# Kernel tuning notes

Hardware: AMD Instinct MI355X
Metric: run time of the kernel (lower is better)

The kernel has to match this reference:

```python
import jax, jax.numpy as jnp
import numpy as np

# ModernBERT-base, local (sliding-window) attention layer (layer_id=1, global every 3)
B, S, H = 2, 4096, 768
NH, HD = 12, 64          # num heads, head dim
WINDOW = 128             # config.local_attention -> +/- WINDOW//2 tokens
ROPE_THETA = 10000.0     # local rope theta
NEG = jnp.float32(-1e9)


def setup_inputs() -> dict:
    key = jax.random.key(0)
    k1, k2, k3 = jax.random.split(key, 3)
    hidden_states = jax.random.normal(k1, (B, S, H), dtype=jnp.float32)
    Wqkv = jax.random.normal(k2, (3 * H, H), dtype=jnp.float32) * 0.02
    Wo = jax.random.normal(k3, (H, H), dtype=jnp.float32) * 0.02
    position_ids = jnp.broadcast_to(jnp.arange(S, dtype=jnp.int32), (B, S))
    # additive masks, [1,1,S,S] broadcast over batch/heads
    attention_mask = jnp.zeros((1, 1, S, S), dtype=jnp.float32)  # full attention (all visible)
    idx = jnp.arange(S)
    dist = jnp.abs(idx[:, None] - idx[None, :])
    sliding_window_mask = jnp.where(dist <= WINDOW // 2, 0.0, NEG).astype(jnp.float32)[None, None]
    return {
        "hidden_states": hidden_states,
        "attention_mask": attention_mask,
        "sliding_window_mask": sliding_window_mask,
        "position_ids": position_ids,
        "Wqkv": Wqkv,
        "Wo": Wo,
    }


def _rope_cos_sin(position_ids):
    inv_freq = 1.0 / (ROPE_THETA ** (jnp.arange(0, HD, 2, dtype=jnp.float32) / HD))  # [HD/2]
    freqs = position_ids.astype(jnp.float32)[..., None] * inv_freq  # [B,S,HD/2]
    emb = jnp.concatenate([freqs, freqs], axis=-1)  # [B,S,HD]
    return jnp.cos(emb), jnp.sin(emb)


def _rotate_half(x):
    x1, x2 = jnp.split(x, 2, axis=-1)
    return jnp.concatenate([-x2, x1], axis=-1)


def reference(hidden_states, attention_mask, sliding_window_mask, position_ids, Wqkv, Wo):
    qkv = jnp.einsum('bsh,oh->bso', hidden_states, Wqkv)  # [B,S,3H]
    q, k, v = jnp.split(qkv, 3, axis=-1)
    q = q.reshape(B, S, NH, HD)
    k = k.reshape(B, S, NH, HD)
    v = v.reshape(B, S, NH, HD)
    cos, sin = _rope_cos_sin(position_ids)  # [B,S,HD]
    cos, sin = cos[:, :, None, :], sin[:, :, None, :]
    q = q * cos + _rotate_half(q) * sin
    k = k * cos + _rotate_half(k) * sin
    # layer_id=1 -> sliding window (local) layer
    mask = sliding_window_mask
    scale = 1.0 / jnp.sqrt(jnp.float32(HD))
    scores = jnp.einsum('bqnd,bknd->bnqk', q, k) * scale + mask  # [B,NH,S,S]
    probs = jax.nn.softmax(scores, axis=-1)
    attn = jnp.einsum('bnqk,bknd->bqnd', probs, v).reshape(B, S, H)
    out = jnp.einsum('bsh,oh->bso', attn, Wo)  # dropout p=0 (eval)
    return out
```

## Files before the change

### kernel.cpp

```cpp
#include <hip/hip_runtime.h>
#include <hip/hip_bf16.h>
#include <math.h>

#define BB 2
#define SS 4096
#define HH 768
#define NHEADS 12
#define MTOT (BB*SS)
#define NQKV (3*HH)

typedef _Float16 f16;
typedef __attribute__((ext_vector_type(8))) _Float16 f16x8;
typedef __attribute__((ext_vector_type(4))) _Float16 f16x4;
typedef __attribute__((ext_vector_type(4))) float f32x4;

__device__ __forceinline__ void gld_lds16(const void* g, void* l) {
  __builtin_amdgcn_global_load_lds(
      (const __attribute__((address_space(1))) unsigned int*)g,
      (__attribute__((address_space(3))) unsigned int*)l, 16, 0, 0);
}

__global__ __launch_bounds__(256)
void cvt_all(const float* __restrict__ hs, const float* __restrict__ wq,
             const float* __restrict__ wo, f16* __restrict__ hs16,
             f16* __restrict__ wq16, f16* __restrict__ wo16) {
  const int n1 = MTOT * HH / 4, n2 = NQKV * HH / 4, n3 = HH * HH / 4;
  int i = blockIdx.x * 256 + threadIdx.x;
  const float* src;
  f16* dst;
  int j = i;
  if (i < n1) { src = hs; dst = hs16; }
  else if (i < n1 + n2) { src = wq; dst = wq16; j = i - n1; }
  else if (i < n1 + n2 + n3) { src = wo; dst = wo16; j = i - n1 - n2; }
  else return;
  float4 v = reinterpret_cast<const float4*>(src)[j];
  f16x4 o;
  o[0] = (f16)v.x; o[1] = (f16)v.y; o[2] = (f16)v.z; o[3] = (f16)v.w;
  reinterpret_cast<f16x4*>(dst)[j] = o;
}

__global__ void rope_table_kernel(float* __restrict__ ctab, float* __restrict__ stab) {
  int idx = blockIdx.x * 256 + threadIdx.x;
  if (idx >= SS * 32) return;
  int s = idx >> 5;
  int j = idx & 31;
  const double r = 0.7498942093324559;
  double inv = 1.0;
  for (int t = 0; t < j; ++t) inv *= r;
  double ph = (double)s * inv;
  const double TWO_PI = 6.283185307179586;
  double red = ph - TWO_PI * floor(ph / TWO_PI);
  float rf = (float)red;
  ctab[idx] = cosf(rf);
  stab[idx] = sinf(rf);
}

template<int EPI>
__global__ __launch_bounds__(256)
void gemm_f16(const f16* __restrict__ A, const f16* __restrict__ Bw,
              float* __restrict__ C,
              f16* __restrict__ Oq, f16* __restrict__ Ok, f16* __restrict__ Ov,
              const int* __restrict__ pos,
              const float* __restrict__ ctab, const float* __restrict__ stab,
              int Mtiles, int N, int K) {
  __shared__ __align__(16) f16 As[3][128][32];
  __shared__ __align__(16) f16 Bs[3][128][32];
  const int tid = threadIdx.x;
  const int lane = tid & 63;
  const int w = tid >> 6;
  const int wr = w >> 1, wc = w & 1;

  const int bid = blockIdx.x;
  const int xcd = bid & 7;
  const int idx = bid >> 3;
  const int mch = Mtiles >> 3;
  const int bm = (xcd * mch + (idx % mch)) * 128;
  const int bn = (idx / mch) * 128;

  f32x4 acc[4][4] = {};

  const int l4 = lane >> 2;
  const int lk = lane & 3;
  const int srow = w * 32;
  const int fr = lane & 15;
  const int fst = (l4 >> 1) & 3;
  const int pc = (((lane >> 4) ^ ((fr >> 1) & 3)) * 8);

  auto stage = [&](int buf, int k0) {
#pragma unroll
    for (int i = 0; i < 2; ++i) {
      int row = srow + i * 16 + l4;
      gld_lds16(A + (size_t)(bm + row) * K + k0 + (lk ^ fst) * 8,
                (char*)&As[0][0][0] + buf * 8192 + w * 2048 + i * 1024 + lane * 16);
      gld_lds16(Bw + (size_t)(bn + row) * K + k0 + (lk ^ fst) * 8,
                (char*)&Bs[0][0][0] + buf * 8192 + w * 2048 + i * 1024 + lane * 16);
    }
  };
  auto compute = [&](int buf) {
    f16x8 av[4], bv[4];
#pragma unroll
    for (int m = 0; m < 4; ++m)
      av[m] = *reinterpret_cast<const f16x8*>(&As[buf][wr * 64 + m * 16 + fr][pc]);
#pragma unroll
    for (int n = 0; n < 4; ++n)
      bv[n] = *reinterpret_cast<const f16x8*>(&Bs[buf][wc * 64 + n * 16 + fr][pc]);
    __builtin_amdgcn_s_setprio(1);
#pragma unroll
    for (int m = 0; m < 4; ++m)
#pragma unroll
      for (int n = 0; n < 4; ++n)
        acc[m][n] = __builtin_amdgcn_mfma_f32_16x16x32_f16(av[m], bv[n],
                                                           acc[m][n], 0, 0, 0);
    __builtin_amdgcn_s_setprio(0);
  };

  const int T = K >> 5;
  stage(0, 0);
  stage(1, 32);
  for (int t = 0; t < T; ++t) {
    if (t == T - 1)
      asm volatile("s_waitcnt vmcnt(0)" ::: "memory");
    else
      asm volatile("s_waitcnt vmcnt(4)" ::: "memory");
    __builtin_amdgcn_s_barrier();
    __builtin_amdgcn_sched_barrier(0);
    if (t + 2 < T) stage((t + 2) % 3, (t + 2) << 5);
    compute(t % 3);
  }

  const int cl = lane & 15;
  const int rg = lane >> 4;
  if (EPI == 0) {
#pragma unroll
    for (int m = 0; m < 4; ++m)
#pragma unroll
      for (int n = 0; n < 4; ++n)
#pragma unroll
        for (int r = 0; r < 4; ++r) {
          int row = bm + wr * 64 + m * 16 + rg * 4 + r;
          int col = bn + wc * 64 + n * 16 + cl;
          C[(size_t)row * N + col] = acc[m][n][r];
        }
  } else {
    const int sec = bn / HH;
    f16* dst = (sec == 0) ? Oq : ((sec == 1) ? Ok : Ov);
    const int hb = bn - sec * HH + wc * 64;
#pragma unroll
    for (int m = 0; m < 4; ++m)
#pragma unroll
      for (int r = 0; r < 4; ++r) {
        int row = bm + wr * 64 + m * 16 + rg * 4 + r;
        if (sec < 2) {
          int s = pos[row];
#pragma unroll
          for (int n = 0; n < 4; ++n) {
            int hd = hb + n * 16 + cl;
            int d = hd & 63;
            int d2 = d & 31;
            float c = ctab[s * 32 + d2];
            float sn = stab[s * 32 + d2];
            float val = acc[m][n][r];
            float pv = acc[m][n ^ 2][r];
            val = (d < 32) ? (val * c - pv * sn) : (val * c + pv * sn);
            if (sec == 0) val *= 0.125f;
            dst[(size_t)row * HH + hd] = (f16)val;
          }
        } else {
#pragma unroll
          for (int n = 0; n < 4; ++n)
            dst[(size_t)row * HH + hb + n * 16 + cl] = (f16)acc[m][n][r];
        }
      }
  }
}

#define AQT 64
#define AKT 192
#define KP 72
#define VPP 200

__global__ __launch_bounds__(256)
void attn_kernel(const f16* __restrict__ qg, const f16* __restrict__ kg,
                 const f16* __restrict__ vg, f16* __restrict__ og) {
  __shared__ __align__(16) f16 Ks[AKT][KP];
  __shared__ __align__(16) f16 Vs[64][192];
  __shared__ float sums[AQT];

  const int tid = threadIdx.x;
  const int lane = tid & 63;
  const int wq = tid >> 6;
  const int l15 = lane & 15, g = lane >> 4;
  const int lin = (blockIdx.x & 7) * 192 + (blockIdx.x >> 3);
  const int qt = lin & 63;
  const int h = (lin >> 6) % NHEADS;
  const int b = lin / (64 * NHEADS);
  const int q0 = qt * AQT;
  const int kbase = q0 - 64;

  const size_t qrow = ((size_t)(b * SS + q0 + wq * 16 + l15)) * HH + h * 64;
  const f16x8 bq0 = *reinterpret_cast<const f16x8*>(&qg[qrow + g * 8]);
  const f16x8 bq1 = *reinterpret_cast<const f16x8*>(&qg[qrow + 32 + g * 8]);

#pragma unroll
  for (int i = 0; i < 6; ++i) {
    int idx = tid + i * 256;
    int r = idx >> 3, ch = idx & 7;
    int kglob = kbase + r;
    f16x8 v = {};
    if (kglob >= 0 && kglob < SS)
      v = *reinterpret_cast<const f16x8*>(
          &kg[((size_t)(b * SS + kglob)) * HH + h * 64 + ch * 8]);
    *reinterpret_cast<f16x8*>(&Ks[r][ch * 8]) = v;
  }
#pragma unroll
  for (int i = 0; i < 6; ++i) {
    int idx = tid + i * 256;
    int r = idx >> 3, ch = idx & 7;
    int kglob = kbase + r;
    f16x8 v = {};
    if (kglob >= 0 && kglob < SS)
      v = *reinterpret_cast<const f16x8*>(
          &vg[((size_t)(b * SS + kglob)) * HH + h * 64 + ch * 8]);
    const int c = r >> 3, o = r & 7;
#pragma unroll
    for (int j = 0; j < 8; ++j) {
      const int row = ch * 8 + j;
      const int cp = c ^ (row & 7) ^ ((row >> 3) & 7);
      Vs[row][cp * 8 + o] = v[j];
    }
  }
  __syncthreads();

  f32x4 accs[12] = {};
#pragma unroll
  for (int f = 0; f < 12; ++f) {
    f16x8 ak = *reinterpret_cast<const f16x8*>(&Ks[f * 16 + l15][g * 8]);
    accs[f] = __builtin_amdgcn_mfma_f32_16x16x32_f16(ak, bq0, accs[f], 0, 0, 0);
  }
#pragma unroll
  for (int f = 0; f < 12; ++f) {
    f16x8 ak = *reinterpret_cast<const f16x8*>(&Ks[f * 16 + l15][32 + g * 8]);
    accs[f] = __builtin_amdgcn_mfma_f32_16x16x32_f16(ak, bq1, accs[f], 0, 0, 0);
  }
  __syncthreads();

  const int qloc = wq * 16 + l15;
  float mx = -1e30f;
#pragma unroll
  for (int f = 0; f < 12; ++f)
#pragma unroll
    for (int r = 0; r < 4; ++r) {
      int key = f * 16 + g * 4 + r;
      int kglob = kbase + key;
      bool valid = (key >= qloc) && (key <= qloc + 128) && (kglob >= 0) && (kglob < SS);
      float s = valid ? accs[f][r] : -1e30f;
      accs[f][r] = s;
      mx = fmaxf(mx, s);
    }
  mx = fmaxf(mx, __shfl_xor(mx, 16));
  mx = fmaxf(mx, __shfl_xor(mx, 32));
  f16* Ps = &Ks[0][0];
  float sum = 0.f;
#pragma unroll
  for (int f = 0; f < 12; ++f) {
    float p0 = __expf(accs[f][0] - mx);
    float p1 = __expf(accs[f][1] - mx);
    float p2 = __expf(accs[f][2] - mx);
    float p3 = __expf(accs[f][3] - mx);
    sum += (p0 + p1) + (p2 + p3);
    f16x4 pk;
    pk[0] = (f16)p0; pk[1] = (f16)p1; pk[2] = (f16)p2; pk[3] = (f16)p3;
    *reinterpret_cast<f16x4*>(&Ps[(size_t)qloc * VPP + f * 16 + g * 4]) = pk;
  }
  sum += __shfl_xor(sum, 16);
  sum += __shfl_xor(sum, 32);
  if (g == 0) sums[qloc] = sum;

  f32x4 acco[4] = {};
#pragma unroll
  for (int ks = 0; ks < 6; ++ks) {
    f16x8 pa = *reinterpret_cast<const f16x8*>(&Ps[(size_t)(wq * 16 + l15) * VPP + ks * 32 + g * 8]);
#pragma unroll
    for (int n = 0; n < 4; ++n) {
      const int row = n * 16 + l15;
      const int cp = (4 * ks + g) ^ (row & 7) ^ ((row >> 3) & 7);
      f16x8 bv = *reinterpret_cast<const f16x8*>(&Vs[row][cp * 8]);
      acco[n] = __builtin_amdgcn_mfma_f32_16x16x32_f16(pa, bv, acco[n], 0, 0, 0);
    }
  }
#pragma unroll
  for (int r = 0; r < 4; ++r) {
    int qo = wq * 16 + g * 4 + r;
    float inv = 1.0f / sums[qo];
    size_t base = ((size_t)(b * SS + q0 + qo)) * HH + h * 64;
#pragma unroll
    for (int n = 0; n < 4; ++n)
      og[base + n * 16 + l15] = (f16)(acco[n][r] * inv);
  }
}

extern "C" void kernel_launch(void* const* d_in, const int* in_sizes, int n_in,
                              void* d_out, int out_size, void* d_ws, size_t ws_size,
                              hipStream_t stream) {
  const float* hs = (const float*)d_in[0];
  const int* pos = (const int*)d_in[3];
  const float* Wqkv = (const float*)d_in[4];
  const float* Wo = (const float*)d_in[5];
  float* out = (float*)d_out;

  uint8_t* ws = (uint8_t*)d_ws;
  size_t off = 0;
  float* ctab = (float*)(ws + off); off += (size_t)SS * 32 * 4;
  float* stab = (float*)(ws + off); off += (size_t)SS * 32 * 4;
  f16* hs16 = (f16*)(ws + off); off += (size_t)MTOT * HH * 2;
  f16* wq16 = (f16*)(ws + off); off += (size_t)NQKV * HH * 2;
  f16* wo16 = (f16*)(ws + off); off += (size_t)HH * HH * 2;
  f16* qf = (f16*)(ws + off); off += (size_t)MTOT * HH * 2;
  f16* kf = (f16*)(ws + off); off += (size_t)MTOT * HH * 2;
  f16* vf = (f16*)(ws + off); off += (size_t)MTOT * HH * 2;
  f16* af = (f16*)(ws + off); off += (size_t)MTOT * HH * 2;

  const int ncvt = (MTOT * HH + NQKV * HH + HH * HH) / 4;
  cvt_all<<<(ncvt + 255) / 256, 256, 0, stream>>>(hs, Wqkv, Wo, hs16, wq16, wo16);
  rope_table_kernel<<<(SS * 32 + 255) / 256, 256, 0, stream>>>(ctab, stab);

  gemm_f16<1><<<(MTOT / 128) * (NQKV / 128), 256, 0, stream>>>(
      hs16, wq16, nullptr, qf, kf, vf, pos, ctab, stab, MTOT / 128, NQKV, HH);
  attn_kernel<<<BB * NHEADS * (SS / AQT), 256, 0, stream>>>(qf, kf, vf, af);
  gemm_f16<0><<<(MTOT / 128) * (HH / 128), 256, 0, stream>>>(
      af, wo16, out, nullptr, nullptr, nullptr, nullptr, nullptr, nullptr,
      MTOT / 128, HH, HH);
}
```

Before: 108.7 us.

## Load GEMM B operand directly into registers instead of staging through LDS

The weight (B) tiles in the f16 GEMM are now read straight from global memory into per-wave registers with double-buffered register sets. Only the A tiles still go through the triple-buffered LDS, which halves shared memory use and removes the B LDS reads. The cost is duplicated global loads of B across the two wave rows, more register pressure, and a new unrolled-by-two pipeline with different wait counts.

```diff
diff --git a/kernel.cpp b/kernel.cpp
--- a/kernel.cpp
+++ b/kernel.cpp
@@ -64,7 +64,6 @@
               const float* __restrict__ ctab, const float* __restrict__ stab,
               int Mtiles, int N, int K) {
   __shared__ __align__(16) f16 As[3][128][32];
-  __shared__ __align__(16) f16 Bs[3][128][32];
   const int tid = threadIdx.x;
   const int lane = tid & 63;
   const int w = tid >> 6;
@@ -83,27 +82,30 @@
   const int lk = lane & 3;
   const int srow = w * 32;
   const int fr = lane & 15;
+  const int g16 = lane >> 4;
   const int fst = (l4 >> 1) & 3;
-  const int pc = (((lane >> 4) ^ ((fr >> 1) & 3)) * 8);
-
-  auto stage = [&](int buf, int k0) {
+  const int pc = ((g16 ^ ((fr >> 1) & 3)) * 8);
+
+  const f16* bp = Bw + (size_t)(bn + wc * 64 + fr) * K + g16 * 8;
+
+  auto stageA = [&](int buf, int k0) {
 #pragma unroll
     for (int i = 0; i < 2; ++i) {
       int row = srow + i * 16 + l4;
       gld_lds16(A + (size_t)(bm + row) * K + k0 + (lk ^ fst) * 8,
                 (char*)&As[0][0][0] + buf * 8192 + w * 2048 + i * 1024 + lane * 16);
-      gld_lds16(Bw + (size_t)(bn + row) * K + k0 + (lk ^ fst) * 8,
-                (char*)&Bs[0][0][0] + buf * 8192 + w * 2048 + i * 1024 + lane * 16);
     }
   };
-  auto compute = [&](int buf) {
-    f16x8 av[4], bv[4];
+  auto loadB = [&](f16x8* breg, int k0) {
+#pragma unroll
+    for (int n = 0; n < 4; ++n)
+      breg[n] = *reinterpret_cast<const f16x8*>(bp + (size_t)n * 16 * K + k0);
+  };
+  auto compute = [&](int abuf, const f16x8* bv) {
+    f16x8 av[4];
 #pragma unroll
     for (int m = 0; m < 4; ++m)
-      av[m] = *reinterpret_cast<const f16x8*>(&As[buf][wr * 64 + m * 16 + fr][pc]);
-#pragma unroll
-    for (int n = 0; n < 4; ++n)
-      bv[n] = *reinterpret_cast<const f16x8*>(&Bs[buf][wc * 64 + n * 16 + fr][pc]);
+      av[m] = *reinterpret_cast<const f16x8*>(&As[abuf][wr * 64 + m * 16 + fr][pc]);
     __builtin_amdgcn_s_setprio(1);
 #pragma unroll
     for (int m = 0; m < 4; ++m)
@@ -115,17 +117,30 @@
   };
 
   const int T = K >> 5;
-  stage(0, 0);
-  stage(1, 32);
-  for (int t = 0; t < T; ++t) {
-    if (t == T - 1)
+  f16x8 b0[4], b1[4];
+  stageA(0, 0);
+  loadB(b0, 0);
+  for (int t = 0; t < T; t += 2) {
+    if (t + 1 < T) {
+      stageA((t + 1) % 3, (t + 1) << 5);
+      loadB(b1, (t + 1) << 5);
+      asm volatile("s_waitcnt vmcnt(6)" ::: "memory");
+    } else {
       asm volatile("s_waitcnt vmcnt(0)" ::: "memory");
-    else
-      asm volatile("s_waitcnt vmcnt(4)" ::: "memory");
+    }
     __builtin_amdgcn_s_barrier();
     __builtin_amdgcn_sched_barrier(0);
-    if (t + 2 < T) stage((t + 2) % 3, (t + 2) << 5);
-    compute(t % 3);
+    compute(t % 3, b0);
+    if (t + 2 < T) {
+      stageA((t + 2) % 3, (t + 2) << 5);
+      loadB(b0, (t + 2) << 5);
+      asm volatile("s_waitcnt vmcnt(6)" ::: "memory");
+    } else {
+      asm volatile("s_waitcnt vmcnt(0)" ::: "memory");
+    }
+    __builtin_amdgcn_s_barrier();
+    __builtin_amdgcn_sched_barrier(0);
+    compute((t + 1) % 3, b1);
   }
 
   const int cl = lane & 15;
```

After: 138.2 us. +27.1%, slower.

## Use 256x128 tiles with 512 threads and double buffering for QKV GEMM

Applied to the files above, without the earlier changes.

The QKV projection GEMM moves into its own kernel with 256x128 output tiles computed by 8 waves (512 threads) instead of 128x128 with 4 waves. The pipeline goes from three LDS buffers to two, adding a barrier after each compute step. The bigger M tile lets each B tile be reused by twice as many rows, cutting global and LDS traffic per FLOP. The cost is half as many blocks (576 instead of 1152) and a shallower prefetch pipeline. The output GEMM is split out unchanged.

```diff
diff --git a/kernel.cpp b/kernel.cpp
--- a/kernel.cpp
+++ b/kernel.cpp
@@ -55,14 +55,115 @@
   stab[idx] = sinf(rf);
 }
 
-template<int EPI>
+__global__ __launch_bounds__(512)
+void gemm1_f16(const f16* __restrict__ A, const f16* __restrict__ Bw,
+               f16* __restrict__ Oq, f16* __restrict__ Ok, f16* __restrict__ Ov,
+               const int* __restrict__ pos,
+               const float* __restrict__ ctab, const float* __restrict__ stab) {
+  __shared__ __align__(16) f16 As[2][256][32];
+  __shared__ __align__(16) f16 Bs[2][128][32];
+  const int K = HH;
+  const int tid = threadIdx.x;
+  const int lane = tid & 63;
+  const int w = tid >> 6;
+  const int wr = w >> 1, wc = w & 1;
+
+  const int bid = blockIdx.x;
+  const int xcd = bid & 7;
+  const int idx = bid >> 3;
+  const int bm = (xcd * 4 + (idx & 3)) * 256;
+  const int bn = (idx >> 2) * 128;
+
+  f32x4 acc[4][4] = {};
+
+  const int l4 = lane >> 2;
+  const int lk = lane & 3;
+  const int fr = lane & 15;
+  const int fst = (l4 >> 1) & 3;
+  const int pc = (((lane >> 4) ^ ((fr >> 1) & 3)) * 8);
+
+  auto stage = [&](int buf, int k0) {
+#pragma unroll
+    for (int i = 0; i < 2; ++i) {
+      int row = w * 32 + i * 16 + l4;
+      gld_lds16(A + (size_t)(bm + row) * K + k0 + (lk ^ fst) * 8,
+                (char*)&As[0][0][0] + buf * 16384 + w * 2048 + i * 1024 + lane * 16);
+    }
+    {
+      int row = w * 16 + l4;
+      gld_lds16(Bw + (size_t)(bn + row) * K + k0 + (lk ^ fst) * 8,
+                (char*)&Bs[0][0][0] + buf * 8192 + w * 1024 + lane * 16);
+    }
+  };
+  auto compute = [&](int buf) {
+    f16x8 av[4], bv[4];
+#pragma unroll
+    for (int m = 0; m < 4; ++m)
+      av[m] = *reinterpret_cast<const f16x8*>(&As[buf][wr * 64 + m * 16 + fr][pc]);
+#pragma unroll
+    for (int n = 0; n < 4; ++n)
+      bv[n] = *reinterpret_cast<const f16x8*>(&Bs[buf][wc * 64 + n * 16 + fr][pc]);
+    __builtin_amdgcn_s_setprio(1);
+#pragma unroll
+    for (int m = 0; m < 4; ++m)
+#pragma unroll
+      for (int n = 0; n < 4; ++n)
+        acc[m][n] = __builtin_amdgcn_mfma_f32_16x16x32_f16(av[m], bv[n],
+                                                           acc[m][n], 0, 0, 0);
+    __builtin_amdgcn_s_setprio(0);
+  };
+
+  const int T = K >> 5;
+  stage(0, 0);
+  for (int t = 0; t < T; ++t) {
+    if (t + 1 < T) {
+      stage((t + 1) & 1, (t + 1) << 5);
+      asm volatile("s_waitcnt vmcnt(3)" ::: "memory");
+    } else {
+      asm volatile("s_waitcnt vmcnt(0)" ::: "memory");
+    }
+    __builtin_amdgcn_s_barrier();
+    __builtin_amdgcn_sched_barrier(0);
+    compute(t & 1);
+    __builtin_amdgcn_s_barrier();
+  }
+
+  const int cl = lane & 15;
+  const int rg = lane >> 4;
+  const int sec = bn / HH;
+  f16* dst = (sec == 0) ? Oq : ((sec == 1) ? Ok : Ov);
+  const int hb = bn - sec * HH + wc * 64;
+#pragma unroll
+  for (int m = 0; m < 4; ++m)
+#pragma unroll
+    for (int r = 0; r < 4; ++r) {
+      const int row = bm + wr * 64 + m * 16 + rg * 4 + r;
+      if (sec < 2) {
+        const int sp = pos[row];
+#pragma unroll
+        for (int n = 0; n < 4; ++n) {
+          const int hd = hb + n * 16 + cl;
+          const int d = hd & 63;
+          const int d2 = d & 31;
+          const float c = ctab[sp * 32 + d2];
+          const float sn = stab[sp * 32 + d2];
+          float val = acc[m][n][r];
+          const float pv = acc[m][n ^ 2][r];
+          val = (d < 32) ? (val * c - pv * sn) : (val * c + pv * sn);
+          if (sec == 0) val *= 0.125f;
+          dst[(size_t)row * HH + hd] = (f16)val;
+        }
+      } else {
+#pragma unroll
+        for (int n = 0; n < 4; ++n)
+          dst[(size_t)row * HH + hb + n * 16 + cl] = (f16)acc[m][n][r];
+      }
+    }
+}
+
 __global__ __launch_bounds__(256)
-void gemm_f16(const f16* __restrict__ A, const f16* __restrict__ Bw,
-              float* __restrict__ C,
-              f16* __restrict__ Oq, f16* __restrict__ Ok, f16* __restrict__ Ov,
-              const int* __restrict__ pos,
-              const float* __restrict__ ctab, const float* __restrict__ stab,
-              int Mtiles, int N, int K) {
+void gemm2_f16(const f16* __restrict__ A, const f16* __restrict__ Bw,
+               float* __restrict__ C, int Mtiles, int N, int K) {
   __shared__ __align__(16) f16 As[3][128][32];
   __shared__ __align__(16) f16 Bs[3][128][32];
   const int tid = threadIdx.x;
@@ -130,48 +231,16 @@
 
   const int cl = lane & 15;
   const int rg = lane >> 4;
-  if (EPI == 0) {
-#pragma unroll
-    for (int m = 0; m < 4; ++m)
-#pragma unroll
-      for (int n = 0; n < 4; ++n)
-#pragma unroll
-        for (int r = 0; r < 4; ++r) {
-          int row = bm + wr * 64 + m * 16 + rg * 4 + r;
-          int col = bn + wc * 64 + n * 16 + cl;
-          C[(size_t)row * N + col] = acc[m][n][r];
-        }
-  } else {
-    const int sec = bn / HH;
-    f16* dst = (sec == 0) ? Oq : ((sec == 1) ? Ok : Ov);
-    const int hb = bn - sec * HH + wc * 64;
-#pragma unroll
-    for (int m = 0; m < 4; ++m)
+#pragma unroll
+  for (int m = 0; m < 4; ++m)
+#pragma unroll
+    for (int n = 0; n < 4; ++n)
 #pragma unroll
       for (int r = 0; r < 4; ++r) {
         int row = bm + wr * 64 + m * 16 + rg * 4 + r;
-        if (sec < 2) {
-          int s = pos[row];
-#pragma unroll
-          for (int n = 0; n < 4; ++n) {
-            int hd = hb + n * 16 + cl;
-            int d = hd & 63;
-            int d2 = d & 31;
-            float c = ctab[s * 32 + d2];
-            float sn = stab[s * 32 + d2];
-            float val = acc[m][n][r];
-            float pv = acc[m][n ^ 2][r];
-            val = (d < 32) ? (val * c - pv * sn) : (val * c + pv * sn);
-            if (sec == 0) val *= 0.125f;
-            dst[(size_t)row * HH + hd] = (f16)val;
-          }
-        } else {
-#pragma unroll
-          for (int n = 0; n < 4; ++n)
-            dst[(size_t)row * HH + hb + n * 16 + cl] = (f16)acc[m][n][r];
-        }
+        int col = bn + wc * 64 + n * 16 + cl;
+        C[(size_t)row * N + col] = acc[m][n][r];
       }
-  }
 }
 
 #define AQT 64
@@ -324,10 +393,9 @@
   cvt_all<<<(ncvt + 255) / 256, 256, 0, stream>>>(hs, Wqkv, Wo, hs16, wq16, wo16);
   rope_table_kernel<<<(SS * 32 + 255) / 256, 256, 0, stream>>>(ctab, stab);
 
-  gemm_f16<1><<<(MTOT / 128) * (NQKV / 128), 256, 0, stream>>>(
-      hs16, wq16, nullptr, qf, kf, vf, pos, ctab, stab, MTOT / 128, NQKV, HH);
+  gemm1_f16<<<(MTOT / 256) * (NQKV / 128), 512, 0, stream>>>(
+      hs16, wq16, qf, kf, vf, pos, ctab, stab);
   attn_kernel<<<BB * NHEADS * (SS / AQT), 256, 0, stream>>>(qf, kf, vf, af);
-  gemm_f16<0><<<(MTOT / 128) * (HH / 128), 256, 0, stream>>>(
-      af, wo16, out, nullptr, nullptr, nullptr, nullptr, nullptr, nullptr,
-      MTOT / 128, HH, HH);
-}
+  gemm2_f16<<<(MTOT / 128) * (HH / 128), 256, 0, stream>>>(
+      af, wo16, out, MTOT / 128, HH, HH);
+}
```

Result: no change. 109.0 us (+0.2%).

## Use 256x128 GEMM tiles with 512 threads, double buffering, and fuse prep kernels

Applied to the files above, without the earlier changes.

Replaces the 128x128, 256-thread GEMM with a 256x128 tile run by 8 waves, so each B tile is reused across twice as many rows. The LDS pipeline drops from triple to double buffering and waits for all loads every iteration. The separate conversion and RoPE-table kernels are merged into one launch to save a kernel launch. The tradeoffs are fewer, larger workgroups (occupancy and load-balance risk across 256 CUs) and less prefetch depth, since the full vmcnt(0) wait exposes more memory latency.

```diff
diff --git a/kernel.cpp b/kernel.cpp
--- a/kernel.cpp
+++ b/kernel.cpp
@@ -21,50 +21,50 @@
 }
 
 __global__ __launch_bounds__(256)
-void cvt_all(const float* __restrict__ hs, const float* __restrict__ wq,
-             const float* __restrict__ wo, f16* __restrict__ hs16,
-             f16* __restrict__ wq16, f16* __restrict__ wo16) {
+void prep_all(const float* __restrict__ hs, const float* __restrict__ wq,
+              const float* __restrict__ wo, f16* __restrict__ hs16,
+              f16* __restrict__ wq16, f16* __restrict__ wo16,
+              float* __restrict__ ctab, float* __restrict__ stab) {
   const int n1 = MTOT * HH / 4, n2 = NQKV * HH / 4, n3 = HH * HH / 4;
+  const int n4 = SS * 32;
   int i = blockIdx.x * 256 + threadIdx.x;
-  const float* src;
-  f16* dst;
-  int j = i;
-  if (i < n1) { src = hs; dst = hs16; }
-  else if (i < n1 + n2) { src = wq; dst = wq16; j = i - n1; }
-  else if (i < n1 + n2 + n3) { src = wo; dst = wo16; j = i - n1 - n2; }
-  else return;
-  float4 v = reinterpret_cast<const float4*>(src)[j];
-  f16x4 o;
-  o[0] = (f16)v.x; o[1] = (f16)v.y; o[2] = (f16)v.z; o[3] = (f16)v.w;
-  reinterpret_cast<f16x4*>(dst)[j] = o;
-}
-
-__global__ void rope_table_kernel(float* __restrict__ ctab, float* __restrict__ stab) {
-  int idx = blockIdx.x * 256 + threadIdx.x;
-  if (idx >= SS * 32) return;
-  int s = idx >> 5;
-  int j = idx & 31;
-  const double r = 0.7498942093324559;
-  double inv = 1.0;
-  for (int t = 0; t < j; ++t) inv *= r;
-  double ph = (double)s * inv;
-  const double TWO_PI = 6.283185307179586;
-  double red = ph - TWO_PI * floor(ph / TWO_PI);
-  float rf = (float)red;
-  ctab[idx] = cosf(rf);
-  stab[idx] = sinf(rf);
-}
-
-template<int EPI>
-__global__ __launch_bounds__(256)
-void gemm_f16(const f16* __restrict__ A, const f16* __restrict__ Bw,
-              float* __restrict__ C,
-              f16* __restrict__ Oq, f16* __restrict__ Ok, f16* __restrict__ Ov,
-              const int* __restrict__ pos,
-              const float* __restrict__ ctab, const float* __restrict__ stab,
-              int Mtiles, int N, int K) {
-  __shared__ __align__(16) f16 As[3][128][32];
-  __shared__ __align__(16) f16 Bs[3][128][32];
+  if (i < n1 + n2 + n3) {
+    const float* src;
+    f16* dst;
+    int j = i;
+    if (i < n1) { src = hs; dst = hs16; }
+    else if (i < n1 + n2) { src = wq; dst = wq16; j = i - n1; }
+    else { src = wo; dst = wo16; j = i - n1 - n2; }
+    float4 v = reinterpret_cast<const float4*>(src)[j];
+    f16x4 o;
+    o[0] = (f16)v.x; o[1] = (f16)v.y; o[2] = (f16)v.z; o[3] = (f16)v.w;
+    reinterpret_cast<f16x4*>(dst)[j] = o;
+  } else if (i < n1 + n2 + n3 + n4) {
+    int idx = i - n1 - n2 - n3;
+    int s = idx >> 5;
+    int j = idx & 31;
+    const double r = 0.7498942093324559;
+    double inv = 1.0;
+    for (int t = 0; t < j; ++t) inv *= r;
+    double ph = (double)s * inv;
+    const double TWO_PI = 6.283185307179586;
+    double red = ph - TWO_PI * floor(ph / TWO_PI);
+    float rf = (float)red;
+    ctab[idx] = cosf(rf);
+    stab[idx] = sinf(rf);
+  }
+}
+
+template<int EPI, int NN>
+__global__ __launch_bounds__(512)
+void gemm_256x128(const f16* __restrict__ A, const f16* __restrict__ Bw,
+                  float* __restrict__ C,
+                  f16* __restrict__ Oq, f16* __restrict__ Ok, f16* __restrict__ Ov,
+                  const int* __restrict__ pos,
+                  const float* __restrict__ ctab, const float* __restrict__ stab) {
+  __shared__ __align__(16) f16 As[2][256][32];
+  __shared__ __align__(16) f16 Bs[2][128][32];
+  const int K = HH;
   const int tid = threadIdx.x;
   const int lane = tid & 63;
   const int w = tid >> 6;
@@ -73,15 +73,13 @@
   const int bid = blockIdx.x;
   const int xcd = bid & 7;
   const int idx = bid >> 3;
-  const int mch = Mtiles >> 3;
-  const int bm = (xcd * mch + (idx % mch)) * 128;
-  const int bn = (idx / mch) * 128;
+  const int bm = (xcd * 4 + (idx & 3)) * 256;
+  const int bn = (idx >> 2) * 128;
 
   f32x4 acc[4][4] = {};
 
   const int l4 = lane >> 2;
   const int lk = lane & 3;
-  const int srow = w * 32;
   const int fr = lane & 15;
   const int fst = (l4 >> 1) & 3;
   const int pc = (((lane >> 4) ^ ((fr >> 1) & 3)) * 8);
@@ -89,11 +87,14 @@
   auto stage = [&](int buf, int k0) {
 #pragma unroll
     for (int i = 0; i < 2; ++i) {
-      int row = srow + i * 16 + l4;
+      int row = w * 32 + i * 16 + l4;
       gld_lds16(A + (size_t)(bm + row) * K + k0 + (lk ^ fst) * 8,
-                (char*)&As[0][0][0] + buf * 8192 + w * 2048 + i * 1024 + lane * 16);
+                (char*)&As[0][0][0] + buf * 16384 + w * 2048 + i * 1024 + lane * 16);
+    }
+    {
+      int row = w * 16 + l4;
       gld_lds16(Bw + (size_t)(bn + row) * K + k0 + (lk ^ fst) * 8,
-                (char*)&Bs[0][0][0] + buf * 8192 + w * 2048 + i * 1024 + lane * 16);
+                (char*)&Bs[0][0][0] + buf * 8192 + w * 1024 + lane * 16);
     }
   };
   auto compute = [&](int buf) {
@@ -116,16 +117,12 @@
 
   const int T = K >> 5;
   stage(0, 0);
-  stage(1, 32);
   for (int t = 0; t < T; ++t) {
-    if (t == T - 1)
-      asm volatile("s_waitcnt vmcnt(0)" ::: "memory");
-    else
-      asm volatile("s_waitcnt vmcnt(4)" ::: "memory");
+    asm volatile("s_waitcnt vmcnt(0)" ::: "memory");
     __builtin_amdgcn_s_barrier();
     __builtin_amdgcn_sched_barrier(0);
-    if (t + 2 < T) stage((t + 2) % 3, (t + 2) << 5);
-    compute(t % 3);
+    if (t + 1 < T) stage((t + 1) & 1, (t + 1) << 5);
+    compute(t & 1);
   }
 
   const int cl = lane & 15;
@@ -139,7 +136,7 @@
         for (int r = 0; r < 4; ++r) {
           int row = bm + wr * 64 + m * 16 + rg * 4 + r;
           int col = bn + wc * 64 + n * 16 + cl;
-          C[(size_t)row * N + col] = acc[m][n][r];
+          C[(size_t)row * NN + col] = acc[m][n][r];
         }
   } else {
     const int sec = bn / HH;
@@ -149,18 +146,18 @@
     for (int m = 0; m < 4; ++m)
 #pragma unroll
       for (int r = 0; r < 4; ++r) {
-        int row = bm + wr * 64 + m * 16 + rg * 4 + r;
+        const int row = bm + wr * 64 + m * 16 + rg * 4 + r;
         if (sec < 2) {
-          int s = pos[row];
+          const int sp = pos[row];
 #pragma unroll
           for (int n = 0; n < 4; ++n) {
-            int hd = hb + n * 16 + cl;
-            int d = hd & 63;
-            int d2 = d & 31;
-            float c = ctab[s * 32 + d2];
-            float sn = stab[s * 32 + d2];
+            const int hd = hb + n * 16 + cl;
+            const int d = hd & 63;
+            const int d2 = d & 31;
+            const float c = ctab[sp * 32 + d2];
+            const float sn = stab[sp * 32 + d2];
             float val = acc[m][n][r];
-            float pv = acc[m][n ^ 2][r];
+            const float pv = acc[m][n ^ 2][r];
             val = (d < 32) ? (val * c - pv * sn) : (val * c + pv * sn);
             if (sec == 0) val *= 0.125f;
             dst[(size_t)row * HH + hd] = (f16)val;
@@ -320,14 +317,13 @@
   f16* vf = (f16*)(ws + off); off += (size_t)MTOT * HH * 2;
   f16* af = (f16*)(ws + off); off += (size_t)MTOT * HH * 2;
 
-  const int ncvt = (MTOT * HH + NQKV * HH + HH * HH) / 4;
-  cvt_all<<<(ncvt + 255) / 256, 256, 0, stream>>>(hs, Wqkv, Wo, hs16, wq16, wo16);
-  rope_table_kernel<<<(SS * 32 + 255) / 256, 256, 0, stream>>>(ctab, stab);
-
-  gemm_f16<1><<<(MTOT / 128) * (NQKV / 128), 256, 0, stream>>>(
-      hs16, wq16, nullptr, qf, kf, vf, pos, ctab, stab, MTOT / 128, NQKV, HH);
+  const int nprep = (MTOT * HH + NQKV * HH + HH * HH) / 4 + SS * 32;
+  prep_all<<<(nprep + 255) / 256, 256, 0, stream>>>(hs, Wqkv, Wo, hs16, wq16,
+                                                    wo16, ctab, stab);
+
+  gemm_256x128<1, NQKV><<<(MTOT / 256) * (NQKV / 128), 512, 0, stream>>>(
+      hs16, wq16, nullptr, qf, kf, vf, pos, ctab, stab);
   attn_kernel<<<BB * NHEADS * (SS / AQT), 256, 0, stream>>>(qf, kf, vf, af);
-  gemm_f16<0><<<(MTOT / 128) * (HH / 128), 256, 0, stream>>>(
-      af, wo16, out, nullptr, nullptr, nullptr, nullptr, nullptr, nullptr,
-      MTOT / 128, HH, HH);
-}
+  gemm_256x128<0, HH><<<(MTOT / 256) * (HH / 128), 512, 0, stream>>>(
+      af, wo16, out, nullptr, nullptr, nullptr, nullptr, nullptr, nullptr);
+}
```

After: 112.2 us. 1.03x slower.
